# Kernel optimization log

Hardware: AMD Instinct MI355X
Metric: run time of the kernel (lower is better)

The kernel has to match this reference:

```python
import jax, jax.numpy as jnp
import numpy as np

B, N, D, FF = 4096, 8, 256, 2048
EPS = 1e-5


def _layernorm(x, gamma, beta):
    mu = jnp.mean(x, axis=-1, keepdims=True)
    var = jnp.mean((x - mu) ** 2, axis=-1, keepdims=True)
    return (x - mu) * jax.lax.rsqrt(var + EPS) * gamma + beta


def _tt_product(x, w):
    # x: [b, d_in, n], w: [d_in, d_out, n]
    # h[:, :, k] = sum_i x[:, :, i] @ w[:, :, (k - i) % n]  (circular contraction)
    n = x.shape[-1]
    k = jnp.arange(n)
    idx = (k[:, None] - k[None, :]) % n          # [k, i]
    wg = w[:, :, idx]                            # [d_in, d_out, k, i]
    return jnp.einsum('bdi,doki->bok', x, wg)    # [b, d_out, n]


def setup_inputs() -> dict:
    key = jax.random.key(0)
    ks = jax.random.split(key, 12)
    xav = lambda k, shp, fi, fo: jax.random.uniform(k, shp, jnp.float32, -1.0, 1.0) * np.sqrt(6.0 / (fi + fo))
    return {
        'ent_seq': jax.random.normal(ks[0], (B, N, D), jnp.float32),
        'w_in': xav(ks[1], (D, D, N), D, D),
        'w_out': xav(ks[2], (D, D, N), D, D),
        'W1': xav(ks[3], (FF, D), D, FF),
        'bias1': jnp.zeros((FF,), jnp.float32),
        'W2': xav(ks[4], (D, FF), FF, D),
        'bias2': jnp.zeros((D,), jnp.float32),
        'gamma1': jnp.ones((D,), jnp.float32),
        'beta1': jnp.zeros((D,), jnp.float32),
        'gamma2': jnp.ones((D,), jnp.float32),
        'beta2': jnp.zeros((D,), jnp.float32),
    }


def reference(ent_seq, w_in, w_out, W1, bias1, W2, bias2, gamma1, beta1, gamma2, beta2):
    # self-attention-like block (dropout = identity in eval mode)
    xn = _layernorm(ent_seq, gamma1, beta1)          # [B, N, D]
    xp = jnp.transpose(xn, (0, 2, 1))                # [B, D, N]
    half = xp.shape[0] // 2
    h = jnp.concatenate([_tt_product(xp[:half], w_in),
                         _tt_product(xp[half:], w_out)], axis=0)
    x = ent_seq + jnp.transpose(h, (0, 2, 1))        # residual
    # FFN block
    yn = _layernorm(x, gamma2, beta2)
    ff = jax.nn.relu(yn @ W1.T + bias1) @ W2.T + bias2
    return x + ff
```

## Files before the change

kernel.cpp:

```cpp
#include <hip/hip_runtime.h>
#include <hip/hip_bf16.h>

typedef unsigned short ushort_t;
typedef __attribute__((ext_vector_type(8))) short bf16x8;
typedef __attribute__((ext_vector_type(4))) float f32x4;

#define B_SZ 4096
#define N_SZ 8
#define D_SZ 256
#define FF_SZ 2048
#define M_SZ (B_SZ * N_SZ)
#define WELEM (D_SZ * D_SZ * N_SZ)

__device__ inline float b2f(ushort_t u) {
    union { unsigned int i; float f; } t; t.i = ((unsigned int)u) << 16; return t.f;
}
__device__ inline ushort_t f2b(float f) {
    union { unsigned int i; float f; } t; t.f = f;
    unsigned int i = t.i;
    unsigned int r = (i + 0x7fffu + ((i >> 16) & 1u)) >> 16;
    return (ushort_t)r;
}

__device__ inline void gl2lds16(const ushort_t* g, ushort_t* l) {
    __builtin_amdgcn_global_load_lds((const __attribute__((address_space(1))) void*)g,
                                     (__attribute__((address_space(3))) void*)l, 16, 0, 0);
}

__global__ __launch_bounds__(256) void convert_weights(const float* __restrict__ w_in,
                                                       const float* __restrict__ w_out,
                                                       const float* __restrict__ W1,
                                                       const float* __restrict__ W2,
                                                       ushort_t* __restrict__ bt_in,
                                                       ushort_t* __restrict__ bt_out,
                                                       ushort_t* __restrict__ W1b,
                                                       ushort_t* __restrict__ W2b) {
    __shared__ float tile[64][65];
    const int bid = blockIdx.x;
    const int t = threadIdx.x;
    if (bid < 256) {
        const float* w = (bid < 128) ? w_in : w_out;
        ushort_t* bt = (bid < 128) ? bt_in : bt_out;
        const int id = bid & 127;
        const int d10 = (id >> 5) * 64;
        const int j0  = (id & 31) * 64;
#pragma unroll
        for (int it = 0; it < 16; ++it) {
            const int d1l = it * 4 + (t >> 6);
            const int jl = t & 63;
            tile[d1l][jl] = w[(size_t)(d10 + d1l) * 2048 + j0 + jl];
        }
        __syncthreads();
#pragma unroll
        for (int it = 0; it < 16; ++it) {
            const int jl = it * 4 + (t >> 6);
            const int d1l = t & 63;
            const int j = j0 + jl;
            bt[(size_t)(j >> 3) * 2048 + (j & 7) * 256 + d10 + d1l] = f2b(tile[d1l][jl]);
        }
    } else {
        const int id = bid - 256;
        const float* w = (id < 256) ? W1 : W2;
        ushort_t* o = (id < 256) ? W1b : W2b;
        const size_t base = (size_t)(id & 255) * 2048 + t * 8;
        const float4 a = *(const float4*)&w[base];
        const float4 b = *(const float4*)&w[base + 4];
        *(ushort4*)&o[base]     = make_ushort4(f2b(a.x), f2b(a.y), f2b(a.z), f2b(a.w));
        *(ushort4*)&o[base + 4] = make_ushort4(f2b(b.x), f2b(b.y), f2b(b.z), f2b(b.w));
    }
}

__global__ __launch_bounds__(256) void ln_fast(const float* __restrict__ xin,
                                               const float* __restrict__ gam,
                                               const float* __restrict__ bet,
                                               ushort_t* __restrict__ out) {
    const int wave = threadIdx.x >> 6;
    const int lane = threadIdx.x & 63;
    const size_t row = (size_t)blockIdx.x * 4 + wave;
    const float4 v = *(const float4*)&xin[row * 256 + lane * 4];
    float s = v.x + v.y + v.z + v.w;
    float q = v.x * v.x + v.y * v.y + v.z * v.z + v.w * v.w;
#pragma unroll
    for (int off = 1; off < 64; off <<= 1) {
        s += __shfl_xor(s, off, 64);
        q += __shfl_xor(q, off, 64);
    }
    const float mu = s * (1.0f / 256.0f);
    const float var = q * (1.0f / 256.0f) - mu * mu;
    const float rs = rsqrtf(var + 1e-5f);
    const float4 g = *(const float4*)&gam[lane * 4];
    const float4 b = *(const float4*)&bet[lane * 4];
    ushort4 o;
    o.x = f2b((v.x - mu) * rs * g.x + b.x);
    o.y = f2b((v.y - mu) * rs * g.y + b.y);
    o.z = f2b((v.z - mu) * rs * g.z + b.z);
    o.w = f2b((v.w - mu) * rs * g.w + b.w);
    *(ushort4*)&out[row * 256 + lane * 4] = o;
}

__global__ __launch_bounds__(256, 2) void tt_ln2(const ushort_t* __restrict__ A,
                                                 const ushort_t* __restrict__ Bt0,
                                                 const ushort_t* __restrict__ Bt1,
                                                 const float* __restrict__ g2,
                                                 const float* __restrict__ be2,
                                                 const float* __restrict__ entf,
                                                 ushort_t* __restrict__ yn,
                                                 ushort_t* __restrict__ xb) {
    __shared__ __attribute__((aligned(16))) ushort_t As[64 * 64];
    __shared__ __attribute__((aligned(16))) ushort_t Bs[256 * 64];
    __shared__ float red_s[64 * 4];
    __shared__ float red_q[64 * 4];

    const int t = threadIdx.x;
    const int lb = ((blockIdx.x & 1) << 8) | (blockIdx.x >> 1);
    const int m0 = lb * 64;
    const int lane = t & 63;
    const int wc = t >> 6;
    const int l16 = lane & 15, quad = lane >> 4;
    const int tr = t >> 3;
    const int csw = (((t & 7) ^ (tr & 7)) << 3);

    const ushort_t* Bt = (m0 >= M_SZ / 2) ? Bt1 : Bt0;

    f32x4 acc[4][4];
#pragma unroll
    for (int i = 0; i < 4; i++)
#pragma unroll
        for (int j = 0; j < 4; j++) acc[i][j] = (f32x4)(0.0f);

#pragma unroll 1
    for (int kt = 0; kt < 32; ++kt) {
        const int kg = kt * 64;
        __syncthreads();
#pragma unroll
        for (int p = 0; p < 2; ++p) {
            const int mrow = m0 + p * 32 + tr;
            const int kcol = kg + csw;
            const int s = kcol >> 8;
            const ushort_t* gA = A + (size_t)((mrow & ~7) + (((mrow & 7) - s) & 7)) * 256 + (kcol & 255);
            gl2lds16(gA, As + p * 2048 + t * 8);
        }
#pragma unroll
        for (int p = 0; p < 8; ++p) {
            gl2lds16(Bt + (size_t)(p * 32 + tr) * 2048 + kg + csw, Bs + p * 2048 + t * 8);
        }
        __syncthreads();

#pragma unroll
        for (int kk = 0; kk < 2; ++kk) {
            const int ac = ((((kk << 2) | quad) ^ (l16 & 7)) << 3);
            bf16x8 af[4], bfv[4];
#pragma unroll
            for (int i = 0; i < 4; i++) af[i]  = *(const bf16x8*)&As[(i * 16 + l16) * 64 + ac];
#pragma unroll
            for (int j = 0; j < 4; j++) bfv[j] = *(const bf16x8*)&Bs[(wc * 64 + j * 16 + l16) * 64 + ac];
#pragma unroll
            for (int i = 0; i < 4; i++)
#pragma unroll
                for (int j = 0; j < 4; j++)
                    acc[i][j] = __builtin_amdgcn_mfma_f32_16x16x32_bf16(af[i], bfv[j], acc[i][j], 0, 0, 0);
        }
    }

    int c[4];
#pragma unroll
    for (int j = 0; j < 4; j++) c[j] = wc * 64 + j * 16 + l16;
#pragma unroll
    for (int i = 0; i < 4; i++) {
#pragma unroll
        for (int r = 0; r < 4; r++) {
            const int rl = i * 16 + quad * 4 + r;
            const size_t grow = (size_t)(m0 + rl) * 256;
            float s = 0.0f, q = 0.0f;
#pragma unroll
            for (int j = 0; j < 4; j++) {
                float v = acc[i][j][r] + entf[grow + c[j]];
                acc[i][j][r] = v;
                s += v;
                q += v * v;
            }
#pragma unroll
            for (int off = 1; off < 16; off <<= 1) {
                s += __shfl_xor(s, off, 64);
                q += __shfl_xor(q, off, 64);
            }
            if (l16 == 0) { red_s[rl * 4 + wc] = s; red_q[rl * 4 + wc] = q; }
        }
    }
    __syncthreads();
#pragma unroll
    for (int i = 0; i < 4; i++) {
#pragma unroll
        for (int r = 0; r < 4; r++) {
            const int rl = i * 16 + quad * 4 + r;
            const size_t grow = (size_t)(m0 + rl) * 256;
            const float4 ss = *(const float4*)&red_s[rl * 4];
            const float4 qq = *(const float4*)&red_q[rl * 4];
            const float S = ss.x + ss.y + ss.z + ss.w;
            const float Q = qq.x + qq.y + qq.z + qq.w;
            const float mu = S * (1.0f / 256.0f);
            const float var = Q * (1.0f / 256.0f) - mu * mu;
            const float rs = rsqrtf(var + 1e-5f);
#pragma unroll
            for (int j = 0; j < 4; j++) {
                const float v = acc[i][j][r];
                yn[grow + c[j]] = f2b((v - mu) * rs * g2[c[j]] + be2[c[j]]);
                xb[grow + c[j]] = f2b(v);
            }
        }
    }
}

__global__ __launch_bounds__(256, 2) void ff_fused(const ushort_t* __restrict__ yn,
                                                   const ushort_t* __restrict__ W1b,
                                                   const ushort_t* __restrict__ W2b,
                                                   const float* __restrict__ bias1,
                                                   const float* __restrict__ bias2,
                                                   const ushort_t* __restrict__ xb,
                                                   float* __restrict__ out) {
    __shared__ __attribute__((aligned(16))) ushort_t As[64 * 64];
    __shared__ __attribute__((aligned(16))) ushort_t Bs[256 * 64];
    __shared__ __attribute__((aligned(16))) ushort_t Hc[64 * 256];

    const int t = threadIdx.x;
    const int m0 = blockIdx.x * 64;
    const int lane = t & 63;
    const int wc = t >> 6;
    const int l16 = lane & 15, quad = lane >> 4;
    const int tr = t >> 3;
    const int csw = (((t & 7) ^ (tr & 7)) << 3);

    f32x4 acc2[4][4];
#pragma unroll
    for (int i = 0; i < 4; i++)
#pragma unroll
        for (int j = 0; j < 4; j++) acc2[i][j] = (f32x4)(0.0f);

    int c4[4];
#pragma unroll
    for (int j = 0; j < 4; j++) c4[j] = wc * 64 + j * 16 + l16;

#pragma unroll 1
    for (int c = 0; c < 8; ++c) {
        f32x4 acc1[4][4];
#pragma unroll
        for (int i = 0; i < 4; i++)
#pragma unroll
            for (int j = 0; j < 4; j++) acc1[i][j] = (f32x4)(0.0f);

#pragma unroll 1
        for (int kb = 0; kb < 4; ++kb) {
            const int kg = kb * 64;
            __syncthreads();
#pragma unroll
            for (int p = 0; p < 2; ++p)
                gl2lds16(yn + (size_t)(m0 + p * 32 + tr) * 256 + kg + csw, As + p * 2048 + t * 8);
#pragma unroll
            for (int p = 0; p < 8; ++p)
                gl2lds16(W1b + (size_t)(c * 256 + p * 32 + tr) * 256 + kg + csw, Bs + p * 2048 + t * 8);
            __syncthreads();
#pragma unroll
            for (int kk = 0; kk < 2; ++kk) {
                const int ac = ((((kk << 2) | quad) ^ (l16 & 7)) << 3);
                bf16x8 af[4], bfv[4];
#pragma unroll
                for (int i = 0; i < 4; i++) af[i]  = *(const bf16x8*)&As[(i * 16 + l16) * 64 + ac];
#pragma unroll
                for (int j = 0; j < 4; j++) bfv[j] = *(const bf16x8*)&Bs[(wc * 64 + j * 16 + l16) * 64 + ac];
#pragma unroll
                for (int i = 0; i < 4; i++)
#pragma unroll
                    for (int j = 0; j < 4; j++)
                        acc1[i][j] = __builtin_amdgcn_mfma_f32_16x16x32_bf16(af[i], bfv[j], acc1[i][j], 0, 0, 0);
            }
        }

#pragma unroll
        for (int j = 0; j < 4; j++) {
            const float bb = bias1[c * 256 + c4[j]];
#pragma unroll
            for (int i = 0; i < 4; i++) {
                const int rbase = i * 16 + quad * 4;
#pragma unroll
                for (int r = 0; r < 4; r++) {
                    const int row = rbase + r;
                    float v = acc1[i][j][r] + bb;
                    v = v > 0.0f ? v : 0.0f;
                    Hc[row * 256 + (c4[j] ^ ((row & 7) << 3))] = f2b(v);
                }
            }
        }

#pragma unroll 1
        for (int kb = 0; kb < 4; ++kb) {
            __syncthreads();
#pragma unroll
            for (int p = 0; p < 8; ++p)
                gl2lds16(W2b + (size_t)(p * 32 + tr) * 2048 + c * 256 + kb * 64 + csw, Bs + p * 2048 + t * 8);
            __syncthreads();
#pragma unroll
            for (int kk = 0; kk < 2; ++kk) {
                const int ank = kb * 64 + (((kk << 2) | quad) << 3);
                const int ah  = ank ^ ((l16 & 7) << 3);
                const int ac  = ((((kk << 2) | quad) ^ (l16 & 7)) << 3);
                bf16x8 af[4], bfv[4];
#pragma unroll
                for (int i = 0; i < 4; i++) af[i]  = *(const bf16x8*)&Hc[(i * 16 + l16) * 256 + ah];
#pragma unroll
                for (int j = 0; j < 4; j++) bfv[j] = *(const bf16x8*)&Bs[(wc * 64 + j * 16 + l16) * 64 + ac];
#pragma unroll
                for (int i = 0; i < 4; i++)
#pragma unroll
                    for (int j = 0; j < 4; j++)
                        acc2[i][j] = __builtin_amdgcn_mfma_f32_16x16x32_bf16(af[i], bfv[j], acc2[i][j], 0, 0, 0);
            }
        }
    }

#pragma unroll
    for (int j = 0; j < 4; j++) {
        const float b2 = bias2[c4[j]];
#pragma unroll
        for (int i = 0; i < 4; i++) {
            const int rbase = m0 + i * 16 + quad * 4;
#pragma unroll
            for (int r = 0; r < 4; r++) {
                const size_t o = (size_t)(rbase + r) * 256 + c4[j];
                out[o] = acc2[i][j][r] + b2 + b2f(xb[o]);
            }
        }
    }
}

extern "C" void kernel_launch(void* const* d_in, const int* in_sizes, int n_in,
                              void* d_out, int out_size, void* d_ws, size_t ws_size,
                              hipStream_t stream) {
    const float* ent   = (const float*)d_in[0];
    const float* w_in  = (const float*)d_in[1];
    const float* w_out = (const float*)d_in[2];
    const float* W1    = (const float*)d_in[3];
    const float* bias1 = (const float*)d_in[4];
    const float* W2    = (const float*)d_in[5];
    const float* bias2 = (const float*)d_in[6];
    const float* g1    = (const float*)d_in[7];
    const float* be1   = (const float*)d_in[8];
    const float* g2    = (const float*)d_in[9];
    const float* be2   = (const float*)d_in[10];
    float* out = (float*)d_out;

    char* ws = (char*)d_ws;
    ushort_t* xn     = (ushort_t*)ws;
    ushort_t* yn     = (ushort_t*)(ws + 16777216);
    ushort_t* xb     = (ushort_t*)(ws + 2 * 16777216);
    ushort_t* bt_in  = (ushort_t*)(ws + 3 * 16777216);
    ushort_t* bt_out = bt_in + WELEM;
    ushort_t* W1b    = bt_out + WELEM;
    ushort_t* W2b    = W1b + WELEM;

    convert_weights<<<dim3(768), dim3(256), 0, stream>>>(w_in, w_out, W1, W2,
                                                         bt_in, bt_out, W1b, W2b);
    ln_fast<<<dim3(M_SZ / 4), dim3(256), 0, stream>>>(ent, g1, be1, xn);
    tt_ln2<<<dim3(M_SZ / 64), dim3(256), 0, stream>>>(xn, bt_in, bt_out, g2, be2, ent, yn, xb);
    ff_fused<<<dim3(M_SZ / 64), dim3(256), 0, stream>>>(yn, W1b, W2b, bias1, bias2, xb, out);
}
```

Baseline: 244.2 us.

## Split fused FFN into two GEMMs and enlarge M tiles to 128 rows

```diff
diff --git a/kernel.cpp b/kernel.cpp
--- a/kernel.cpp
+++ b/kernel.cpp
@@ -98,22 +98,23 @@
     *(ushort4*)&out[row * 256 + lane * 4] = o;
 }
 
-__global__ __launch_bounds__(256, 2) void tt_ln2(const ushort_t* __restrict__ A,
-                                                 const ushort_t* __restrict__ Bt0,
-                                                 const ushort_t* __restrict__ Bt1,
-                                                 const float* __restrict__ g2,
-                                                 const float* __restrict__ be2,
-                                                 const float* __restrict__ entf,
-                                                 ushort_t* __restrict__ yn,
-                                                 ushort_t* __restrict__ xb) {
-    __shared__ __attribute__((aligned(16))) ushort_t As[64 * 64];
+
+__global__ __launch_bounds__(256, 3) void tt_v3(const ushort_t* __restrict__ A,
+                                                const ushort_t* __restrict__ Bt0,
+                                                const ushort_t* __restrict__ Bt1,
+                                                const float* __restrict__ g2,
+                                                const float* __restrict__ be2,
+                                                const float* __restrict__ entf,
+                                                ushort_t* __restrict__ yn,
+                                                ushort_t* __restrict__ xb) {
+    __shared__ __attribute__((aligned(16))) ushort_t As[128 * 64];
     __shared__ __attribute__((aligned(16))) ushort_t Bs[256 * 64];
-    __shared__ float red_s[64 * 4];
-    __shared__ float red_q[64 * 4];
+    __shared__ float red_s[128 * 4];
+    __shared__ float red_q[128 * 4];
 
     const int t = threadIdx.x;
-    const int lb = ((blockIdx.x & 1) << 8) | (blockIdx.x >> 1);
-    const int m0 = lb * 64;
+    const int lb = ((blockIdx.x & 1) << 7) | (blockIdx.x >> 1);
+    const int m0 = lb * 128;
     const int lane = t & 63;
     const int wc = t >> 6;
     const int l16 = lane & 15, quad = lane >> 4;
@@ -122,9 +123,9 @@
 
     const ushort_t* Bt = (m0 >= M_SZ / 2) ? Bt1 : Bt0;
 
-    f32x4 acc[4][4];
-#pragma unroll
-    for (int i = 0; i < 4; i++)
+    f32x4 acc[8][4];
+#pragma unroll
+    for (int i = 0; i < 8; i++)
 #pragma unroll
         for (int j = 0; j < 4; j++) acc[i][j] = (f32x4)(0.0f);
 
@@ -133,7 +134,7 @@
         const int kg = kt * 64;
         __syncthreads();
 #pragma unroll
-        for (int p = 0; p < 2; ++p) {
+        for (int p = 0; p < 4; ++p) {
             const int mrow = m0 + p * 32 + tr;
             const int kcol = kg + csw;
             const int s = kcol >> 8;
@@ -149,24 +150,24 @@
 #pragma unroll
         for (int kk = 0; kk < 2; ++kk) {
             const int ac = ((((kk << 2) | quad) ^ (l16 & 7)) << 3);
-            bf16x8 af[4], bfv[4];
-#pragma unroll
-            for (int i = 0; i < 4; i++) af[i]  = *(const bf16x8*)&As[(i * 16 + l16) * 64 + ac];
+            bf16x8 af[8], bfv[4];
+#pragma unroll
+            for (int i = 0; i < 8; i++) af[i]  = *(const bf16x8*)&As[(i * 16 + l16) * 64 + ac];
 #pragma unroll
             for (int j = 0; j < 4; j++) bfv[j] = *(const bf16x8*)&Bs[(wc * 64 + j * 16 + l16) * 64 + ac];
 #pragma unroll
-            for (int i = 0; i < 4; i++)
+            for (int i = 0; i < 8; i++)
 #pragma unroll
                 for (int j = 0; j < 4; j++)
                     acc[i][j] = __builtin_amdgcn_mfma_f32_16x16x32_bf16(af[i], bfv[j], acc[i][j], 0, 0, 0);
         }
     }
 
-    int c[4];
-#pragma unroll
-    for (int j = 0; j < 4; j++) c[j] = wc * 64 + j * 16 + l16;
-#pragma unroll
-    for (int i = 0; i < 4; i++) {
+    int c4[4];
+#pragma unroll
+    for (int j = 0; j < 4; j++) c4[j] = wc * 64 + j * 16 + l16;
+#pragma unroll
+    for (int i = 0; i < 8; i++) {
 #pragma unroll
         for (int r = 0; r < 4; r++) {
             const int rl = i * 16 + quad * 4 + r;
@@ -174,7 +175,7 @@
             float s = 0.0f, q = 0.0f;
 #pragma unroll
             for (int j = 0; j < 4; j++) {
-                float v = acc[i][j][r] + entf[grow + c[j]];
+                float v = acc[i][j][r] + entf[grow + c4[j]];
                 acc[i][j][r] = v;
                 s += v;
                 q += v * v;
@@ -189,7 +190,7 @@
     }
     __syncthreads();
 #pragma unroll
-    for (int i = 0; i < 4; i++) {
+    for (int i = 0; i < 8; i++) {
 #pragma unroll
         for (int r = 0; r < 4; r++) {
             const int rl = i * 16 + quad * 4 + r;
@@ -204,129 +205,143 @@
 #pragma unroll
             for (int j = 0; j < 4; j++) {
                 const float v = acc[i][j][r];
-                yn[grow + c[j]] = f2b((v - mu) * rs * g2[c[j]] + be2[c[j]]);
-                xb[grow + c[j]] = f2b(v);
-            }
-        }
-    }
-}
-
-__global__ __launch_bounds__(256, 2) void ff_fused(const ushort_t* __restrict__ yn,
+                yn[grow + c4[j]] = f2b((v - mu) * rs * g2[c4[j]] + be2[c4[j]]);
+                xb[grow + c4[j]] = f2b(v);
+            }
+        }
+    }
+}
+
+__global__ __launch_bounds__(256, 3) void ff_g1_v3(const ushort_t* __restrict__ yn,
                                                    const ushort_t* __restrict__ W1b,
-                                                   const ushort_t* __restrict__ W2b,
                                                    const float* __restrict__ bias1,
-                                                   const float* __restrict__ bias2,
-                                                   const ushort_t* __restrict__ xb,
-                                                   float* __restrict__ out) {
-    __shared__ __attribute__((aligned(16))) ushort_t As[64 * 64];
+                                                   ushort_t* __restrict__ H) {
+    __shared__ __attribute__((aligned(16))) ushort_t As[128 * 64];
     __shared__ __attribute__((aligned(16))) ushort_t Bs[256 * 64];
-    __shared__ __attribute__((aligned(16))) ushort_t Hc[64 * 256];
 
     const int t = threadIdx.x;
-    const int m0 = blockIdx.x * 64;
+    const int ntile = blockIdx.x >> 8;
+    const int mtile = blockIdx.x & 255;
+    const int m0 = mtile * 128;
+    const int n0 = ntile * 256;
     const int lane = t & 63;
     const int wc = t >> 6;
     const int l16 = lane & 15, quad = lane >> 4;
     const int tr = t >> 3;
     const int csw = (((t & 7) ^ (tr & 7)) << 3);
 
-    f32x4 acc2[4][4];
-#pragma unroll
-    for (int i = 0; i < 4; i++)
-#pragma unroll
-        for (int j = 0; j < 4; j++) acc2[i][j] = (f32x4)(0.0f);
-
-    int c4[4];
-#pragma unroll
-    for (int j = 0; j < 4; j++) c4[j] = wc * 64 + j * 16 + l16;
+    f32x4 acc[8][4];
+#pragma unroll
+    for (int i = 0; i < 8; i++)
+#pragma unroll
+        for (int j = 0; j < 4; j++) acc[i][j] = (f32x4)(0.0f);
 
 #pragma unroll 1
-    for (int c = 0; c < 8; ++c) {
-        f32x4 acc1[4][4];
-#pragma unroll
-        for (int i = 0; i < 4; i++)
-#pragma unroll
-            for (int j = 0; j < 4; j++) acc1[i][j] = (f32x4)(0.0f);
+    for (int kt = 0; kt < 4; ++kt) {
+        const int kg = kt * 64;
+        __syncthreads();
+#pragma unroll
+        for (int p = 0; p < 4; ++p)
+            gl2lds16(yn + (size_t)(m0 + p * 32 + tr) * 256 + kg + csw, As + p * 2048 + t * 8);
+#pragma unroll
+        for (int p = 0; p < 8; ++p)
+            gl2lds16(W1b + (size_t)(n0 + p * 32 + tr) * 256 + kg + csw, Bs + p * 2048 + t * 8);
+        __syncthreads();
+
+#pragma unroll
+        for (int kk = 0; kk < 2; ++kk) {
+            const int ac = ((((kk << 2) | quad) ^ (l16 & 7)) << 3);
+            bf16x8 af[8], bfv[4];
+#pragma unroll
+            for (int i = 0; i < 8; i++) af[i]  = *(const bf16x8*)&As[(i * 16 + l16) * 64 + ac];
+#pragma unroll
+            for (int j = 0; j < 4; j++) bfv[j] = *(const bf16x8*)&Bs[(wc * 64 + j * 16 + l16) * 64 + ac];
+#pragma unroll
+            for (int i = 0; i < 8; i++)
+#pragma unroll
+                for (int j = 0; j < 4; j++)
+                    acc[i][j] = __builtin_amdgcn_mfma_f32_16x16x32_bf16(af[i], bfv[j], acc[i][j], 0, 0, 0);
+        }
+    }
+
+#pragma unroll
+    for (int j = 0; j < 4; j++) {
+        const int col = n0 + wc * 64 + j * 16 + l16;
+        const float bb = bias1[col];
+#pragma unroll
+        for (int i = 0; i < 8; i++) {
+            const int rbase = m0 + i * 16 + quad * 4;
+#pragma unroll
+            for (int r = 0; r < 4; r++) {
+                float v = acc[i][j][r] + bb;
+                v = v > 0.0f ? v : 0.0f;
+                H[(size_t)(rbase + r) * 2048 + col] = f2b(v);
+            }
+        }
+    }
+}
+
+__global__ __launch_bounds__(256, 3) void ff_g2_v3(const ushort_t* __restrict__ H,
+                                                   const ushort_t* __restrict__ W2b,
+                                                   const float* __restrict__ bias2,
+                                                   const ushort_t* __restrict__ xb,
+                                                   float* __restrict__ out) {
+    __shared__ __attribute__((aligned(16))) ushort_t As[128 * 64];
+    __shared__ __attribute__((aligned(16))) ushort_t Bs[256 * 64];
+
+    const int t = threadIdx.x;
+    const int m0 = blockIdx.x * 128;
+    const int lane = t & 63;
+    const int wc = t >> 6;
+    const int l16 = lane & 15, quad = lane >> 4;
+    const int tr = t >> 3;
+    const int csw = (((t & 7) ^ (tr & 7)) << 3);
+
+    f32x4 acc[8][4];
+#pragma unroll
+    for (int i = 0; i < 8; i++)
+#pragma unroll
+        for (int j = 0; j < 4; j++) acc[i][j] = (f32x4)(0.0f);
 
 #pragma unroll 1
-        for (int kb = 0; kb < 4; ++kb) {
-            const int kg = kb * 64;
-            __syncthreads();
-#pragma unroll
-            for (int p = 0; p < 2; ++p)
-                gl2lds16(yn + (size_t)(m0 + p * 32 + tr) * 256 + kg + csw, As + p * 2048 + t * 8);
-#pragma unroll
-            for (int p = 0; p < 8; ++p)
-                gl2lds16(W1b + (size_t)(c * 256 + p * 32 + tr) * 256 + kg + csw, Bs + p * 2048 + t * 8);
-            __syncthreads();
-#pragma unroll
-            for (int kk = 0; kk < 2; ++kk) {
-                const int ac = ((((kk << 2) | quad) ^ (l16 & 7)) << 3);
-                bf16x8 af[4], bfv[4];
-#pragma unroll
-                for (int i = 0; i < 4; i++) af[i]  = *(const bf16x8*)&As[(i * 16 + l16) * 64 + ac];
-#pragma unroll
-                for (int j = 0; j < 4; j++) bfv[j] = *(const bf16x8*)&Bs[(wc * 64 + j * 16 + l16) * 64 + ac];
-#pragma unroll
-                for (int i = 0; i < 4; i++)
-#pragma unroll
-                    for (int j = 0; j < 4; j++)
-                        acc1[i][j] = __builtin_amdgcn_mfma_f32_16x16x32_bf16(af[i], bfv[j], acc1[i][j], 0, 0, 0);
-            }
-        }
-
-#pragma unroll
-        for (int j = 0; j < 4; j++) {
-            const float bb = bias1[c * 256 + c4[j]];
-#pragma unroll
-            for (int i = 0; i < 4; i++) {
-                const int rbase = i * 16 + quad * 4;
-#pragma unroll
-                for (int r = 0; r < 4; r++) {
-                    const int row = rbase + r;
-                    float v = acc1[i][j][r] + bb;
-                    v = v > 0.0f ? v : 0.0f;
-                    Hc[row * 256 + (c4[j] ^ ((row & 7) << 3))] = f2b(v);
-                }
-            }
-        }
-
-#pragma unroll 1
-        for (int kb = 0; kb < 4; ++kb) {
-            __syncthreads();
-#pragma unroll
-            for (int p = 0; p < 8; ++p)
-                gl2lds16(W2b + (size_t)(p * 32 + tr) * 2048 + c * 256 + kb * 64 + csw, Bs + p * 2048 + t * 8);
-            __syncthreads();
-#pragma unroll
-            for (int kk = 0; kk < 2; ++kk) {
-                const int ank = kb * 64 + (((kk << 2) | quad) << 3);
-                const int ah  = ank ^ ((l16 & 7) << 3);
-                const int ac  = ((((kk << 2) | quad) ^ (l16 & 7)) << 3);
-                bf16x8 af[4], bfv[4];
-#pragma unroll
-                for (int i = 0; i < 4; i++) af[i]  = *(const bf16x8*)&Hc[(i * 16 + l16) * 256 + ah];
-#pragma unroll
-                for (int j = 0; j < 4; j++) bfv[j] = *(const bf16x8*)&Bs[(wc * 64 + j * 16 + l16) * 64 + ac];
-#pragma unroll
-                for (int i = 0; i < 4; i++)
-#pragma unroll
-                    for (int j = 0; j < 4; j++)
-                        acc2[i][j] = __builtin_amdgcn_mfma_f32_16x16x32_bf16(af[i], bfv[j], acc2[i][j], 0, 0, 0);
-            }
+    for (int kt = 0; kt < 32; ++kt) {
+        const int kg = kt * 64;
+        __syncthreads();
+#pragma unroll
+        for (int p = 0; p < 4; ++p)
+            gl2lds16(H + (size_t)(m0 + p * 32 + tr) * 2048 + kg + csw, As + p * 2048 + t * 8);
+#pragma unroll
+        for (int p = 0; p < 8; ++p)
+            gl2lds16(W2b + (size_t)(p * 32 + tr) * 2048 + kg + csw, Bs + p * 2048 + t * 8);
+        __syncthreads();
+
+#pragma unroll
+        for (int kk = 0; kk < 2; ++kk) {
+            const int ac = ((((kk << 2) | quad) ^ (l16 & 7)) << 3);
+            bf16x8 af[8], bfv[4];
+#pragma unroll
+            for (int i = 0; i < 8; i++) af[i]  = *(const bf16x8*)&As[(i * 16 + l16) * 64 + ac];
+#pragma unroll
+            for (int j = 0; j < 4; j++) bfv[j] = *(const bf16x8*)&Bs[(wc * 64 + j * 16 + l16) * 64 + ac];
+#pragma unroll
+            for (int i = 0; i < 8; i++)
+#pragma unroll
+                for (int j = 0; j < 4; j++)
+                    acc[i][j] = __builtin_amdgcn_mfma_f32_16x16x32_bf16(af[i], bfv[j], acc[i][j], 0, 0, 0);
         }
     }
 
 #pragma unroll
     for (int j = 0; j < 4; j++) {
-        const float b2 = bias2[c4[j]];
-#pragma unroll
-        for (int i = 0; i < 4; i++) {
+        const int col = wc * 64 + j * 16 + l16;
+        const float b2 = bias2[col];
+#pragma unroll
+        for (int i = 0; i < 8; i++) {
             const int rbase = m0 + i * 16 + quad * 4;
 #pragma unroll
             for (int r = 0; r < 4; r++) {
-                const size_t o = (size_t)(rbase + r) * 256 + c4[j];
-                out[o] = acc2[i][j][r] + b2 + b2f(xb[o]);
+                const size_t o = (size_t)(rbase + r) * 256 + col;
+                out[o] = acc[i][j][r] + b2 + b2f(xb[o]);
             }
         }
     }
@@ -356,10 +371,12 @@
     ushort_t* bt_out = bt_in + WELEM;
     ushort_t* W1b    = bt_out + WELEM;
     ushort_t* W2b    = W1b + WELEM;
+    ushort_t* Hbuf   = (ushort_t*)(ws + 54525952);
 
     convert_weights<<<dim3(768), dim3(256), 0, stream>>>(w_in, w_out, W1, W2,
                                                          bt_in, bt_out, W1b, W2b);
     ln_fast<<<dim3(M_SZ / 4), dim3(256), 0, stream>>>(ent, g1, be1, xn);
-    tt_ln2<<<dim3(M_SZ / 64), dim3(256), 0, stream>>>(xn, bt_in, bt_out, g2, be2, ent, yn, xb);
-    ff_fused<<<dim3(M_SZ / 64), dim3(256), 0, stream>>>(yn, W1b, W2b, bias1, bias2, xb, out);
-}
+    tt_v3<<<dim3(M_SZ / 128), dim3(256), 0, stream>>>(xn, bt_in, bt_out, g2, be2, ent, yn, xb);
+    ff_g1_v3<<<dim3((M_SZ / 128) * (FF_SZ / 256)), dim3(256), 0, stream>>>(yn, W1b, bias1, Hbuf);
+    ff_g2_v3<<<dim3(M_SZ / 128), dim3(256), 0, stream>>>(Hbuf, W2b, bias2, xb, out);
+}
```

Result: slower. 441.1 us (+80.6%).

## Rewrite fused FFN kernel as 4-stage pipelined 128-row tile with 8 waves

Applied to the files above, without the earlier changes.

```diff
diff --git a/kernel.cpp b/kernel.cpp
--- a/kernel.cpp
+++ b/kernel.cpp
@@ -25,6 +25,22 @@
 __device__ inline void gl2lds16(const ushort_t* g, ushort_t* l) {
     __builtin_amdgcn_global_load_lds((const __attribute__((address_space(1))) void*)g,
                                      (__attribute__((address_space(3))) void*)l, 16, 0, 0);
+}
+
+#define BAR()     __builtin_amdgcn_s_barrier()
+#define WVC(n)    asm volatile("s_waitcnt vmcnt(" #n ")" ::: "memory")
+#define LGKM0()   asm volatile("s_waitcnt lgkmcnt(0)" ::: "memory")
+
+__device__ __forceinline__ void waitv(int w) {
+    switch (w) {
+        case 0: WVC(0); break;
+        case 2: WVC(2); break;
+        case 4: WVC(4); break;
+        case 6: WVC(6); break;
+        case 7: WVC(7); break;
+        case 8: WVC(8); break;
+        default: WVC(9); break;
+    }
 }
 
 __global__ __launch_bounds__(256) void convert_weights(const float* __restrict__ w_in,
@@ -211,24 +227,26 @@
     }
 }
 
-__global__ __launch_bounds__(256, 2) void ff_fused(const ushort_t* __restrict__ yn,
-                                                   const ushort_t* __restrict__ W1b,
-                                                   const ushort_t* __restrict__ W2b,
-                                                   const float* __restrict__ bias1,
-                                                   const float* __restrict__ bias2,
-                                                   const ushort_t* __restrict__ xb,
-                                                   float* __restrict__ out) {
-    __shared__ __attribute__((aligned(16))) ushort_t As[64 * 64];
-    __shared__ __attribute__((aligned(16))) ushort_t Bs[256 * 64];
-    __shared__ __attribute__((aligned(16))) ushort_t Hc[64 * 256];
+__global__ __launch_bounds__(512, 2) void ff_pipe(const ushort_t* __restrict__ yn,
+                                                  const ushort_t* __restrict__ W1b,
+                                                  const ushort_t* __restrict__ W2b,
+                                                  const float* __restrict__ bias1,
+                                                  const float* __restrict__ bias2,
+                                                  const ushort_t* __restrict__ xb,
+                                                  float* __restrict__ out) {
+    __shared__ __attribute__((aligned(16))) ushort_t As[4][128 * 32];
+    __shared__ __attribute__((aligned(16))) ushort_t Bs[4][256 * 32];
+    __shared__ __attribute__((aligned(16))) ushort_t Hc[128 * 256];
 
     const int t = threadIdx.x;
-    const int m0 = blockIdx.x * 64;
+    const int m0 = blockIdx.x * 128;
     const int lane = t & 63;
-    const int wc = t >> 6;
+    const int wave = t >> 6;
+    const int wr = wave >> 2, wc = wave & 3;
     const int l16 = lane & 15, quad = lane >> 4;
-    const int tr = t >> 3;
-    const int csw = (((t & 7) ^ (tr & 7)) << 3);
+    const int r4 = t >> 2;
+    const int ssl = (t & 3) ^ ((r4 >> 1) & 3);
+    const int aoff = (quad ^ ((l16 >> 1) & 3)) << 3;
 
     f32x4 acc2[4][4];
 #pragma unroll
@@ -240,80 +258,121 @@
 #pragma unroll
     for (int j = 0; j < 4; j++) c4[j] = wc * 64 + j * 16 + l16;
 
-#pragma unroll 1
-    for (int c = 0; c < 8; ++c) {
-        f32x4 acc1[4][4];
+    auto stage_unit = [&](int u) {
+        const int cs = u >> 4, ps = u & 15, q = u & 3;
+        if (ps < 8) {
+            gl2lds16(yn + (size_t)(m0 + r4) * 256 + ps * 32 + ssl * 8, &As[q][t * 8]);
+            gl2lds16(W1b + (size_t)(cs * 256 + r4) * 256 + ps * 32 + ssl * 8, &Bs[q][t * 8]);
+            gl2lds16(W1b + (size_t)(cs * 256 + 128 + r4) * 256 + ps * 32 + ssl * 8, &Bs[q][4096 + t * 8]);
+        } else {
+            const int kb = ps - 8;
+            gl2lds16(W2b + (size_t)r4 * 2048 + cs * 256 + kb * 32 + ssl * 8, &Bs[q][t * 8]);
+            gl2lds16(W2b + (size_t)(128 + r4) * 2048 + cs * 256 + kb * 32 + ssl * 8, &Bs[q][4096 + t * 8]);
+        }
+    };
+
+    auto comp_g1 = [&](int q, f32x4 (&a1)[4][4]) {
+        bf16x8 af[4], bfv[4];
+#pragma unroll
+        for (int i = 0; i < 4; i++) af[i]  = *(const bf16x8*)&As[q][(wr * 64 + i * 16 + l16) * 32 + aoff];
+#pragma unroll
+        for (int j = 0; j < 4; j++) bfv[j] = *(const bf16x8*)&Bs[q][(wc * 64 + j * 16 + l16) * 32 + aoff];
 #pragma unroll
         for (int i = 0; i < 4; i++)
 #pragma unroll
-            for (int j = 0; j < 4; j++) acc1[i][j] = (f32x4)(0.0f);
-
-#pragma unroll 1
-        for (int kb = 0; kb < 4; ++kb) {
-            const int kg = kb * 64;
-            __syncthreads();
-#pragma unroll
-            for (int p = 0; p < 2; ++p)
-                gl2lds16(yn + (size_t)(m0 + p * 32 + tr) * 256 + kg + csw, As + p * 2048 + t * 8);
-#pragma unroll
-            for (int p = 0; p < 8; ++p)
-                gl2lds16(W1b + (size_t)(c * 256 + p * 32 + tr) * 256 + kg + csw, Bs + p * 2048 + t * 8);
-            __syncthreads();
-#pragma unroll
-            for (int kk = 0; kk < 2; ++kk) {
-                const int ac = ((((kk << 2) | quad) ^ (l16 & 7)) << 3);
-                bf16x8 af[4], bfv[4];
-#pragma unroll
-                for (int i = 0; i < 4; i++) af[i]  = *(const bf16x8*)&As[(i * 16 + l16) * 64 + ac];
-#pragma unroll
-                for (int j = 0; j < 4; j++) bfv[j] = *(const bf16x8*)&Bs[(wc * 64 + j * 16 + l16) * 64 + ac];
-#pragma unroll
-                for (int i = 0; i < 4; i++)
-#pragma unroll
-                    for (int j = 0; j < 4; j++)
-                        acc1[i][j] = __builtin_amdgcn_mfma_f32_16x16x32_bf16(af[i], bfv[j], acc1[i][j], 0, 0, 0);
-            }
-        }
-
+            for (int j = 0; j < 4; j++)
+                a1[i][j] = __builtin_amdgcn_mfma_f32_16x16x32_bf16(af[i], bfv[j], a1[i][j], 0, 0, 0);
+    };
+
+    auto comp_g2 = [&](int q, int kb) {
+        const int ah = (kb * 32 + quad * 8) ^ ((l16 & 7) << 3);
+        bf16x8 af[4], bfv[4];
+#pragma unroll
+        for (int i = 0; i < 4; i++) af[i]  = *(const bf16x8*)&Hc[(wr * 64 + i * 16 + l16) * 256 + ah];
+#pragma unroll
+        for (int j = 0; j < 4; j++) bfv[j] = *(const bf16x8*)&Bs[q][(wc * 64 + j * 16 + l16) * 32 + aoff];
+#pragma unroll
+        for (int i = 0; i < 4; i++)
+#pragma unroll
+            for (int j = 0; j < 4; j++)
+                acc2[i][j] = __builtin_amdgcn_mfma_f32_16x16x32_bf16(af[i], bfv[j], acc2[i][j], 0, 0, 0);
+    };
+
+    auto hc_write = [&](int c, f32x4 (&a1)[4][4]) {
 #pragma unroll
         for (int j = 0; j < 4; j++) {
             const float bb = bias1[c * 256 + c4[j]];
 #pragma unroll
             for (int i = 0; i < 4; i++) {
-                const int rbase = i * 16 + quad * 4;
+                const int rbase = wr * 64 + i * 16 + quad * 4;
 #pragma unroll
                 for (int r = 0; r < 4; r++) {
                     const int row = rbase + r;
-                    float v = acc1[i][j][r] + bb;
+                    float v = a1[i][j][r] + bb;
                     v = v > 0.0f ? v : 0.0f;
                     Hc[row * 256 + (c4[j] ^ ((row & 7) << 3))] = f2b(v);
                 }
             }
         }
+        LGKM0();
+    };
+
+    constexpr int WM[16] = {9,9,9,9,9,8,7,6, 6,6,6,6,6,7,8,9};
+    constexpr int W7[16] = {9,9,9,9,9,8,7,6, 6,6,6,6,6,4,2,0};
+
+    stage_unit(0); stage_unit(1); stage_unit(2);
 
 #pragma unroll 1
-        for (int kb = 0; kb < 4; ++kb) {
-            __syncthreads();
-#pragma unroll
-            for (int p = 0; p < 8; ++p)
-                gl2lds16(W2b + (size_t)(p * 32 + tr) * 2048 + c * 256 + kb * 64 + csw, Bs + p * 2048 + t * 8);
-            __syncthreads();
-#pragma unroll
-            for (int kk = 0; kk < 2; ++kk) {
-                const int ank = kb * 64 + (((kk << 2) | quad) << 3);
-                const int ah  = ank ^ ((l16 & 7) << 3);
-                const int ac  = ((((kk << 2) | quad) ^ (l16 & 7)) << 3);
-                bf16x8 af[4], bfv[4];
-#pragma unroll
-                for (int i = 0; i < 4; i++) af[i]  = *(const bf16x8*)&Hc[(i * 16 + l16) * 256 + ah];
-#pragma unroll
-                for (int j = 0; j < 4; j++) bfv[j] = *(const bf16x8*)&Bs[(wc * 64 + j * 16 + l16) * 64 + ac];
-#pragma unroll
-                for (int i = 0; i < 4; i++)
-#pragma unroll
-                    for (int j = 0; j < 4; j++)
-                        acc2[i][j] = __builtin_amdgcn_mfma_f32_16x16x32_bf16(af[i], bfv[j], acc2[i][j], 0, 0, 0);
-            }
+    for (int c = 0; c < 7; ++c) {
+        f32x4 acc1[4][4];
+#pragma unroll
+        for (int i = 0; i < 4; i++)
+#pragma unroll
+            for (int j = 0; j < 4; j++) acc1[i][j] = (f32x4)(0.0f);
+
+        const int u0 = c * 16;
+#pragma unroll
+        for (int p = 0; p < 8; ++p) {
+            BAR();
+            stage_unit(u0 + p + 3);
+            waitv(WM[p]);
+            BAR();
+            comp_g1((u0 + p) & 3, acc1);
+        }
+        hc_write(c, acc1);
+#pragma unroll
+        for (int p = 8; p < 16; ++p) {
+            BAR();
+            stage_unit(u0 + p + 3);
+            waitv(WM[p]);
+            BAR();
+            comp_g2((u0 + p) & 3, p - 8);
+        }
+    }
+    {
+        f32x4 acc1[4][4];
+#pragma unroll
+        for (int i = 0; i < 4; i++)
+#pragma unroll
+            for (int j = 0; j < 4; j++) acc1[i][j] = (f32x4)(0.0f);
+
+        const int u0 = 112;
+#pragma unroll
+        for (int p = 0; p < 8; ++p) {
+            BAR();
+            stage_unit(u0 + p + 3);
+            waitv(W7[p]);
+            BAR();
+            comp_g1((u0 + p) & 3, acc1);
+        }
+        hc_write(7, acc1);
+#pragma unroll
+        for (int p = 8; p < 16; ++p) {
+            BAR();
+            if (p <= 12) stage_unit(u0 + p + 3);
+            waitv(W7[p]);
+            BAR();
+            comp_g2((u0 + p) & 3, p - 8);
         }
     }
 
@@ -322,7 +381,7 @@
         const float b2 = bias2[c4[j]];
 #pragma unroll
         for (int i = 0; i < 4; i++) {
-            const int rbase = m0 + i * 16 + quad * 4;
+            const int rbase = m0 + wr * 64 + i * 16 + quad * 4;
 #pragma unroll
             for (int r = 0; r < 4; r++) {
                 const size_t o = (size_t)(rbase + r) * 256 + c4[j];
@@ -361,5 +420,5 @@
                                                          bt_in, bt_out, W1b, W2b);
     ln_fast<<<dim3(M_SZ / 4), dim3(256), 0, stream>>>(ent, g1, be1, xn);
     tt_ln2<<<dim3(M_SZ / 64), dim3(256), 0, stream>>>(xn, bt_in, bt_out, g2, be2, ent, yn, xb);
-    ff_fused<<<dim3(M_SZ / 64), dim3(256), 0, stream>>>(yn, W1b, W2b, bias1, bias2, xb, out);
-}
+    ff_pipe<<<dim3(M_SZ / 128), dim3(512), 0, stream>>>(yn, W1b, W2b, bias1, bias2, xb, out);
+}
```

Result: slower. 279.6 us (+14.5%).
